# Optimization experiments

Hardware: AMD Instinct MI355X
Metric: run time of the kernel (lower is better)

Reference implementation:

```python
import jax, jax.numpy as jnp
import numpy as np


def setup_inputs() -> dict:
    key = jax.random.key(0)
    ks = jax.random.split(key, 8)
    N, E = 100000, 1600000
    d_in, d_h, d_out = 64, 128, 64
    x = jax.random.normal(ks[0], (N, d_in), dtype=jnp.float32)
    edge_index = jax.random.randint(ks[1], (2, E), 0, N, dtype=jnp.int64)
    def glorot(k, shape):
        lim = float(np.sqrt(6.0 / (shape[0] + shape[1])))
        return jax.random.uniform(k, shape, jnp.float32, -lim, lim)
    return {
        "x": x,
        "edge_index": edge_index,
        "W1": glorot(ks[2], (d_in, d_h)), "b1": jnp.zeros((d_h,), jnp.float32),
        "W2": glorot(ks[3], (d_h, d_h)), "b2": jnp.zeros((d_h,), jnp.float32),
        "W3": glorot(ks[4], (d_h, d_out)), "b3": jnp.zeros((d_out,), jnp.float32),
    }


def _gcn_norm(edge_index, num_nodes):
    # PyG gcn_norm with add_self_loops=True, edge_weight=1
    loops = jnp.arange(num_nodes, dtype=edge_index.dtype)
    src = jnp.concatenate([edge_index[0], loops])
    dst = jnp.concatenate([edge_index[1], loops])
    deg = jax.ops.segment_sum(jnp.ones_like(dst, dtype=jnp.float32), dst,
                              num_segments=num_nodes)
    dis = jnp.where(deg > 0, jax.lax.rsqrt(deg), 0.0)
    norm = dis[src] * dis[dst]  # [E+N]
    return src, dst, norm


def _gcn_layer(h, src, dst, norm, W, b, num_nodes):
    h = h @ W                                   # [N, d_out]
    msg = h[src] * norm[:, None]                # gather + scale
    out = jax.ops.segment_sum(msg, dst, num_segments=num_nodes)
    return out + b


def reference(x, edge_index, W1, b1, W2, b2, W3, b3):
    N = x.shape[0]
    src, dst, norm = _gcn_norm(edge_index, N)
    h = _gcn_layer(x, src, dst, norm, W1, b1, N)
    h = jax.nn.gelu(h, approximate=False)
    h = _gcn_layer(h, src, dst, norm, W2, b2, N)
    h = jax.nn.gelu(h, approximate=False)
    h = _gcn_layer(h, src, dst, norm, W3, b3, N)
    return h
```

## Files before the change

kernel.cpp:

```cpp
#include <hip/hip_runtime.h>
#include <hip/hip_fp16.h>
#include <cstdint>
#include <cstddef>


#define CHUNK 4096
#define BSHIFT 7
#define BSZ 128

typedef _Float16 half8 __attribute__((ext_vector_type(8)));
typedef float floatx4 __attribute__((ext_vector_type(4)));

__device__ __forceinline__ int eload(const int* ei, int elem, int is64) {
  return is64 ? ei[2 * elem] : ei[elem];
}

__global__ void k_detect(const int* __restrict__ ei, int* __restrict__ flag) {
  __shared__ int sh[256];
  int tid = threadIdx.x;
  int o = 0;
  for (int i = tid; i < 1024; i += 256) o |= ei[2 * i + 1];
  sh[tid] = o;
  __syncthreads();
  for (int s = 128; s > 0; s >>= 1) {
    if (tid < s) sh[tid] |= sh[tid + s];
    __syncthreads();
  }
  if (tid == 0) *flag = (sh[0] == 0) ? 1 : 0;
}

__global__ __launch_bounds__(256) void k_hist(const int* __restrict__ ei,
                                              int* __restrict__ hist, int E,
                                              int N, int NBLK,
                                              const int* __restrict__ flag) {
  __shared__ int lh[1024];
  int tid = threadIdx.x;
  int P = (N + BSZ - 1) >> BSHIFT;
  for (int i = tid; i < P; i += 256) lh[i] = 0;
  __syncthreads();
  int is64 = *flag;
  int e0 = blockIdx.x * CHUNK;
  int e1 = min(e0 + CHUNK, E);
  for (int e = e0 + tid; e < e1; e += 256) {
    int d = eload(ei, E + e, is64);
    atomicAdd(&lh[d >> BSHIFT], 1);
  }
  __syncthreads();
  for (int b = tid; b < P; b += 256) hist[b * NBLK + blockIdx.x] = lh[b];
}

__global__ __launch_bounds__(256) void k_scanA(const int* __restrict__ in,
                                               int* __restrict__ out,
                                               int* __restrict__ bsum, int n) {
  __shared__ int sh[256];
  int tid = threadIdx.x;
  int base = blockIdx.x * 1024 + tid * 4;
  int v0 = (base + 0 < n) ? in[base + 0] : 0;
  int v1 = (base + 1 < n) ? in[base + 1] : 0;
  int v2 = (base + 2 < n) ? in[base + 2] : 0;
  int v3 = (base + 3 < n) ? in[base + 3] : 0;
  int tsum = v0 + v1 + v2 + v3;
  sh[tid] = tsum;
  __syncthreads();
  for (int o = 1; o < 256; o <<= 1) {
    int x = (tid >= o) ? sh[tid - o] : 0;
    __syncthreads();
    sh[tid] += x;
    __syncthreads();
  }
  int excl = sh[tid] - tsum;
  if (base + 0 < n) out[base + 0] = excl;
  if (base + 1 < n) out[base + 1] = excl + v0;
  if (base + 2 < n) out[base + 2] = excl + v0 + v1;
  if (base + 3 < n) out[base + 3] = excl + v0 + v1 + v2;
  if (tid == 255) bsum[blockIdx.x] = sh[255];
}

__global__ __launch_bounds__(256) void k_scanB(int* __restrict__ bsum, int NB) {
  __shared__ int sh[256];
  int tid = threadIdx.x;
  int base = tid * 4;
  int v0 = (base + 0 < NB) ? bsum[base + 0] : 0;
  int v1 = (base + 1 < NB) ? bsum[base + 1] : 0;
  int v2 = (base + 2 < NB) ? bsum[base + 2] : 0;
  int v3 = (base + 3 < NB) ? bsum[base + 3] : 0;
  int tsum = v0 + v1 + v2 + v3;
  sh[tid] = tsum;
  __syncthreads();
  for (int o = 1; o < 256; o <<= 1) {
    int x = (tid >= o) ? sh[tid - o] : 0;
    __syncthreads();
    sh[tid] += x;
    __syncthreads();
  }
  int excl = sh[tid] - tsum;
  if (base + 0 < NB) bsum[base + 0] = excl;
  if (base + 1 < NB) bsum[base + 1] = excl + v0;
  if (base + 2 < NB) bsum[base + 2] = excl + v0 + v1;
  if (base + 3 < NB) bsum[base + 3] = excl + v0 + v1 + v2;
}

__global__ __launch_bounds__(256) void k_scanC(int* __restrict__ out,
                                               const int* __restrict__ bsum,
                                               int n, int total) {
  int i = blockIdx.x * 256 + threadIdx.x;
  if (i == 0) out[n] = total;
  if (i < n) out[i] += bsum[i >> 10];
}

__global__ __launch_bounds__(256) void k_scatter(const int* __restrict__ ei,
                                                 const int* __restrict__ histoff,
                                                 int* __restrict__ pairs, int E,
                                                 int N, int NBLK,
                                                 const int* __restrict__ flag) {
  __shared__ int lcur[1024];
  int tid = threadIdx.x;
  int P = (N + BSZ - 1) >> BSHIFT;
  for (int b = tid; b < P; b += 256)
    lcur[b] = histoff[b * NBLK + blockIdx.x];
  __syncthreads();
  int is64 = *flag;
  int e0 = blockIdx.x * CHUNK;
  int e1 = min(e0 + CHUNK, E);
  for (int e = e0 + tid; e < e1; e += 256) {
    int s = eload(ei, e, is64);
    int d = eload(ei, E + e, is64);
    int pos = atomicAdd(&lcur[d >> BSHIFT], 1);
    pairs[pos] = (s << BSHIFT) | (d & (BSZ - 1));
  }
}

__global__ __launch_bounds__(256) void k_build_bucket(
    const int* __restrict__ pairs, const int* __restrict__ histoff,
    int* __restrict__ off, float* __restrict__ dis, int* __restrict__ csr,
    int E, int N, int NBLK, int P) {
  __shared__ int lc[BSZ];
  __shared__ int lscan[BSZ];
  __shared__ int lcur[BSZ];
  int tid = threadIdx.x;
  int b = blockIdx.x;
  if (tid < BSZ) lc[tid] = 0;
  __syncthreads();
  int s0 = histoff[b * NBLK];
  int s1 = histoff[(b + 1) * NBLK];
  for (int i = s0 + tid; i < s1; i += 256)
    atomicAdd(&lc[pairs[i] & (BSZ - 1)], 1);
  __syncthreads();
  if (tid < BSZ) lscan[tid] = lc[tid];
  __syncthreads();
#pragma unroll
  for (int o = 1; o < BSZ; o <<= 1) {
    int v = 0;
    if (tid < BSZ && tid >= o) v = lscan[tid - o];
    __syncthreads();
    if (tid < BSZ) lscan[tid] += v;
    __syncthreads();
  }
  int node = (b << BSHIFT) + tid;
  if (tid < BSZ) {
    int o_node = s0 + lscan[tid] - lc[tid];
    lcur[tid] = o_node;
    if (node < N) {
      off[node] = o_node;
      dis[node] = rsqrtf((float)(lc[tid] + 1));
    }
  }
  if (b == P - 1 && tid == 0) off[N] = E;
  __syncthreads();
  for (int i = s0 + tid; i < s1; i += 256) {
    int pk = pairs[i];
    int pos = atomicAdd(&lcur[pk & (BSZ - 1)], 1);
    csr[pos] = pk >> BSHIFT;
  }
}

__global__ __launch_bounds__(256) void k_scale(const float* __restrict__ x,
                                               const float* __restrict__ dis,
                                               __half* __restrict__ xs, int N) {
  int i = blockIdx.x * 256 + threadIdx.x;
  int total = N * 16;
  if (i < total) {
    float d = dis[i >> 4];
    float4 v = ((const float4*)x)[i];
    union { uint2 u; __half2 h[2]; } pk;
    pk.h[0] = __floats2half2_rn(v.x * d, v.y * d);
    pk.h[1] = __floats2half2_rn(v.z * d, v.w * d);
    ((uint2*)xs)[i] = pk.u;
  }
}

__device__ __forceinline__ float gelu_exact(float v) {
  return 0.5f * v * (1.0f + erff(v * 0.70710678118654752440f));
}

template <int K, int M, int EPI>
__global__ __launch_bounds__(256) void k_gemm5(
    const __half* __restrict__ X, const float* __restrict__ W,
    const float* __restrict__ dis, const float* __restrict__ bias,
    __half* __restrict__ G, int N) {
  constexpr int NT = M / 16;
  constexpr int KK = K / 32;
  __shared__ _Float16 WtL[M * K];

  int tid = threadIdx.x;
  for (int t = tid; t < M * K / 8; t += 256) {
    int l = t & 63;
    int fid = t >> 6;
    int nt = fid / KK, kk = fid % KK;
    int n = nt * 16 + (l & 15);
    int k0 = kk * 32 + (l >> 4) * 8;
    half8 h;
#pragma unroll
    for (int e = 0; e < 8; e++)
      h[e] = (_Float16)W[(size_t)(k0 + e) * M + n];
    *(half8*)&WtL[(size_t)t * 8] = h;
  }
  __syncthreads();

  int wave = tid >> 6, l = tid & 63;
  int lr = l & 15, lg = l >> 4;
  int row0 = blockIdx.x * 64 + wave * 16;

  half8 a[KK];
  {
    int row = min(row0 + lr, N - 1);
    const __half* xp = X + (size_t)row * K + lg * 8;
#pragma unroll
    for (int kk = 0; kk < KK; kk++)
      a[kk] = *(const half8*)(xp + kk * 32);
  }

  floatx4 acc[NT];
#pragma unroll
  for (int nt = 0; nt < NT; nt++) acc[nt] = {0.f, 0.f, 0.f, 0.f};

#pragma unroll
  for (int nt = 0; nt < NT; nt++) {
#pragma unroll
    for (int kk = 0; kk < KK; kk++) {
      half8 b = *(const half8*)&WtL[(size_t)((nt * KK + kk) * 64 + l) * 8];
      acc[nt] = __builtin_amdgcn_mfma_f32_16x16x32_f16(a[kk], b, acc[nt], 0, 0, 0);
    }
  }

#pragma unroll
  for (int r = 0; r < 4; r++) {
    int row = row0 + lg * 4 + r;
    if (row < N) {
      float dd = (EPI == 0) ? dis[row] : 0.f;
#pragma unroll
      for (int nt = 0; nt < NT; nt++) {
        int col = nt * 16 + lr;
        float v = acc[nt][r];
        if constexpr (EPI == 0) v *= dd;
        else v = gelu_exact(v + bias[col]);
        G[(size_t)row * M + col] = __float2half(v);
      }
    }
  }
}

__device__ __forceinline__ void acc8(float* a, uint4 r) {
  const __half2* h = reinterpret_cast<const __half2*>(&r);
#pragma unroll
  for (int q = 0; q < 4; q++) {
    float2 f = __half22float2(h[q]);
    a[2 * q] += f.x;
    a[2 * q + 1] += f.y;
  }
}

template <int D, bool HAS_BIAS, bool HAS_GELU, bool F16OUT>
__global__ __launch_bounds__(256) void k_agg(
    const __half* __restrict__ g, const int* __restrict__ off,
    const int* __restrict__ csr, const float* __restrict__ dis,
    const float* __restrict__ bias, void* __restrict__ outv, int N) {
  constexpr int LPN = D / 8;
  constexpr int NPW = 64 / LPN;
  int wave = (blockIdx.x * 256 + threadIdx.x) >> 6;
  int lane = threadIdx.x & 63;
  int sub = lane / LPN;
  int sl = lane % LPN;
  int node = wave * NPW + sub;
  if (node >= N) return;
  const uint4* G16 = (const uint4*)g;
  float a[8];
#pragma unroll
  for (int q = 0; q < 8; q++) a[q] = 0.f;
  acc8(a, G16[(size_t)node * LPN + sl]);
  int beg = off[node], end = off[node + 1];
  int j = beg;
  for (; j + 4 <= end; j += 4) {
    int s0 = csr[j], s1 = csr[j + 1], s2 = csr[j + 2], s3 = csr[j + 3];
    uint4 r0 = G16[(size_t)s0 * LPN + sl];
    uint4 r1 = G16[(size_t)s1 * LPN + sl];
    uint4 r2 = G16[(size_t)s2 * LPN + sl];
    uint4 r3 = G16[(size_t)s3 * LPN + sl];
    acc8(a, r0);
    acc8(a, r1);
    acc8(a, r2);
    acc8(a, r3);
  }
  for (; j < end; j++) acc8(a, G16[(size_t)csr[j] * LPN + sl]);
  float dd = dis[node];
  int c0 = sl * 8;
  float v[8];
#pragma unroll
  for (int q = 0; q < 8; q++) v[q] = a[q] * dd;
  if constexpr (HAS_BIAS) {
    float4 b0 = *(const float4*)&bias[c0];
    float4 b1 = *(const float4*)&bias[c0 + 4];
    v[0] += b0.x; v[1] += b0.y; v[2] += b0.z; v[3] += b0.w;
    v[4] += b1.x; v[5] += b1.y; v[6] += b1.z; v[7] += b1.w;
  }
  if constexpr (HAS_GELU) {
#pragma unroll
    for (int q = 0; q < 8; q++) v[q] = gelu_exact(v[q]);
  }
  if constexpr (F16OUT) {
    union { uint4 u; __half2 h[4]; } pk;
#pragma unroll
    for (int q = 0; q < 4; q++)
      pk.h[q] = __floats2half2_rn(v[2 * q], v[2 * q + 1]);
    *(uint4*)&((__half*)outv)[(size_t)node * D + c0] = pk.u;
  } else {
    float* out = (float*)outv;
    float4 o0 = {v[0], v[1], v[2], v[3]};
    float4 o1 = {v[4], v[5], v[6], v[7]};
    *(float4*)&out[(size_t)node * D + c0] = o0;
    *(float4*)&out[(size_t)node * D + c0 + 4] = o1;
  }
}

extern "C" void kernel_launch(void* const* d_in, const int* in_sizes, int n_in,
                              void* d_out, int out_size, void* d_ws,
                              size_t ws_size, hipStream_t stream) {
  const float* x = (const float*)d_in[0];
  const int* ei = (const int*)d_in[1];
  const float* W1 = (const float*)d_in[2];
  const float* b1 = (const float*)d_in[3];
  const float* W2 = (const float*)d_in[4];
  const float* b2 = (const float*)d_in[5];
  const float* W3 = (const float*)d_in[6];
  const float* b3 = (const float*)d_in[7];
  float* out = (float*)d_out;

  const int N = in_sizes[0] / 64;
  const int E = in_sizes[1] / 2;

  const int NBLK = (E + CHUNK - 1) / CHUNK;
  const int P = (N + BSZ - 1) >> BSHIFT;
  const int HT = P * NBLK;

  char* p = (char*)d_ws;
  auto alloc = [&](size_t bytes) {
    char* r = p;
    p += (bytes + 255) & ~(size_t)255;
    return r;
  };
  float* dis = (float*)alloc((size_t)N * 4);
  int* off = (int*)alloc((size_t)(N + 1) * 4);
  int* bsumH = (int*)alloc(4096);
  int* flag = (int*)alloc(256);
  int* hist = (int*)alloc((size_t)(HT + 1) * 4);
  int* histoff = (int*)alloc((size_t)(HT + 1) * 4);
  int* pairs = (int*)alloc((size_t)E * 4);
  int* csr = (int*)alloc((size_t)E * 4);
  __half* xsh = (__half*)alloc((size_t)N * 64 * 2);
  __half* Xa_h = (__half*)alloc((size_t)N * 64 * 2);
  __half* h1_h = (__half*)alloc((size_t)N * 128 * 2);
  __half* gh = (__half*)alloc((size_t)N * 128 * 2);
  __half* h2_h = (__half*)alloc((size_t)N * 128 * 2);
  __half* gh2 = (__half*)alloc((size_t)N * 64 * 2);

  const int NBH = (HT + 1023) / 1024;

  k_detect<<<1, 256, 0, stream>>>(ei, flag);
  k_hist<<<NBLK, 256, 0, stream>>>(ei, hist, E, N, NBLK, flag);
  k_scanA<<<NBH, 256, 0, stream>>>(hist, histoff, bsumH, HT);
  k_scanB<<<1, 256, 0, stream>>>(bsumH, NBH);
  k_scanC<<<(HT + 255) / 256, 256, 0, stream>>>(histoff, bsumH, HT, E);
  k_scatter<<<NBLK, 256, 0, stream>>>(ei, histoff, pairs, E, N, NBLK, flag);
  k_build_bucket<<<P, 256, 0, stream>>>(pairs, histoff, off, dis, csr, E, N,
                                        NBLK, P);

  const int gemm_blocks = (N + 63) / 64;
  const int agg128_blocks = (N + 15) / 16;
  const int agg64_blocks = (N + 31) / 32;

  k_scale<<<(N * 16 + 255) / 256, 256, 0, stream>>>(x, dis, xsh, N);
  k_agg<64, false, false, true><<<agg64_blocks, 256, 0, stream>>>(
      xsh, off, csr, dis, nullptr, (void*)Xa_h, N);
  k_gemm5<64, 128, 1><<<gemm_blocks, 256, 0, stream>>>(Xa_h, W1, nullptr, b1,
                                                       h1_h, N);
  k_gemm5<128, 128, 0><<<gemm_blocks, 256, 0, stream>>>(h1_h, W2, dis, nullptr,
                                                        gh, N);
  k_agg<128, true, true, true><<<agg128_blocks, 256, 0, stream>>>(
      gh, off, csr, dis, b2, (void*)h2_h, N);
  k_gemm5<128, 64, 0><<<gemm_blocks, 256, 0, stream>>>(h2_h, W3, dis, nullptr,
                                                       gh2, N);
  k_agg<64, true, false, false><<<agg64_blocks, 256, 0, stream>>>(
      gh2, off, csr, dis, b3, (void*)out, N);
}
```

Baseline: 235.3 us.

## Replace histogram scan chain with atomic bucket offsets and per-block int64 detection

```diff
diff --git a/kernel.cpp b/kernel.cpp
--- a/kernel.cpp
+++ b/kernel.cpp
@@ -15,50 +15,53 @@
   return is64 ? ei[2 * elem] : ei[elem];
 }
 
-__global__ void k_detect(const int* __restrict__ ei, int* __restrict__ flag) {
-  __shared__ int sh[256];
-  int tid = threadIdx.x;
-  int o = 0;
-  for (int i = tid; i < 1024; i += 256) o |= ei[2 * i + 1];
-  sh[tid] = o;
-  __syncthreads();
-  for (int s = 128; s > 0; s >>= 1) {
-    if (tid < s) sh[tid] |= sh[tid + s];
-    __syncthreads();
-  }
-  if (tid == 0) *flag = (sh[0] == 0) ? 1 : 0;
-}
-
-__global__ __launch_bounds__(256) void k_hist(const int* __restrict__ ei,
-                                              int* __restrict__ hist, int E,
-                                              int N, int NBLK,
-                                              const int* __restrict__ flag) {
+__device__ __forceinline__ int detect_is64(const int* ei, int e0, int e1,
+                                           int* lflag) {
+  int tid = threadIdx.x;
+  if (tid == 0) *lflag = 0;
+  __syncthreads();
+  int cnt = min(256, e1 - e0);
+  if (tid < cnt) {
+    if (ei[2 * (e0 + tid) + 1] != 0) atomicOr(lflag, 1);
+  }
+  __syncthreads();
+  return (*lflag == 0) ? 1 : 0;
+}
+
+__global__ __launch_bounds__(256) void k_count(const int* __restrict__ ei,
+                                               int* __restrict__ total,
+                                               int* __restrict__ base_mat,
+                                               int E, int N, int NBLK) {
   __shared__ int lh[1024];
+  __shared__ int lflag;
   int tid = threadIdx.x;
   int P = (N + BSZ - 1) >> BSHIFT;
-  for (int i = tid; i < P; i += 256) lh[i] = 0;
-  __syncthreads();
-  int is64 = *flag;
   int e0 = blockIdx.x * CHUNK;
   int e1 = min(e0 + CHUNK, E);
+  int is64 = detect_is64(ei, e0, e1, &lflag);
+  for (int i = tid; i < P; i += 256) lh[i] = 0;
+  __syncthreads();
   for (int e = e0 + tid; e < e1; e += 256) {
     int d = eload(ei, E + e, is64);
     atomicAdd(&lh[d >> BSHIFT], 1);
   }
   __syncthreads();
-  for (int b = tid; b < P; b += 256) hist[b * NBLK + blockIdx.x] = lh[b];
-}
-
-__global__ __launch_bounds__(256) void k_scanA(const int* __restrict__ in,
-                                               int* __restrict__ out,
-                                               int* __restrict__ bsum, int n) {
+  for (int b = tid; b < P; b += 256) {
+    int c = lh[b];
+    base_mat[(size_t)b * NBLK + blockIdx.x] = c ? atomicAdd(&total[b], c) : 0;
+  }
+}
+
+__global__ __launch_bounds__(256) void k_scanP(const int* __restrict__ total,
+                                               int* __restrict__ base, int P,
+                                               int E) {
   __shared__ int sh[256];
   int tid = threadIdx.x;
-  int base = blockIdx.x * 1024 + tid * 4;
-  int v0 = (base + 0 < n) ? in[base + 0] : 0;
-  int v1 = (base + 1 < n) ? in[base + 1] : 0;
-  int v2 = (base + 2 < n) ? in[base + 2] : 0;
-  int v3 = (base + 3 < n) ? in[base + 3] : 0;
+  int b0 = tid * 4;
+  int v0 = (b0 + 0 < P) ? total[b0 + 0] : 0;
+  int v1 = (b0 + 1 < P) ? total[b0 + 1] : 0;
+  int v2 = (b0 + 2 < P) ? total[b0 + 2] : 0;
+  int v3 = (b0 + 3 < P) ? total[b0 + 3] : 0;
   int tsum = v0 + v1 + v2 + v3;
   sh[tid] = tsum;
   __syncthreads();
@@ -69,59 +72,27 @@
     __syncthreads();
   }
   int excl = sh[tid] - tsum;
-  if (base + 0 < n) out[base + 0] = excl;
-  if (base + 1 < n) out[base + 1] = excl + v0;
-  if (base + 2 < n) out[base + 2] = excl + v0 + v1;
-  if (base + 3 < n) out[base + 3] = excl + v0 + v1 + v2;
-  if (tid == 255) bsum[blockIdx.x] = sh[255];
-}
-
-__global__ __launch_bounds__(256) void k_scanB(int* __restrict__ bsum, int NB) {
-  __shared__ int sh[256];
-  int tid = threadIdx.x;
-  int base = tid * 4;
-  int v0 = (base + 0 < NB) ? bsum[base + 0] : 0;
-  int v1 = (base + 1 < NB) ? bsum[base + 1] : 0;
-  int v2 = (base + 2 < NB) ? bsum[base + 2] : 0;
-  int v3 = (base + 3 < NB) ? bsum[base + 3] : 0;
-  int tsum = v0 + v1 + v2 + v3;
-  sh[tid] = tsum;
-  __syncthreads();
-  for (int o = 1; o < 256; o <<= 1) {
-    int x = (tid >= o) ? sh[tid - o] : 0;
-    __syncthreads();
-    sh[tid] += x;
-    __syncthreads();
-  }
-  int excl = sh[tid] - tsum;
-  if (base + 0 < NB) bsum[base + 0] = excl;
-  if (base + 1 < NB) bsum[base + 1] = excl + v0;
-  if (base + 2 < NB) bsum[base + 2] = excl + v0 + v1;
-  if (base + 3 < NB) bsum[base + 3] = excl + v0 + v1 + v2;
-}
-
-__global__ __launch_bounds__(256) void k_scanC(int* __restrict__ out,
-                                               const int* __restrict__ bsum,
-                                               int n, int total) {
-  int i = blockIdx.x * 256 + threadIdx.x;
-  if (i == 0) out[n] = total;
-  if (i < n) out[i] += bsum[i >> 10];
-}
-
-__global__ __launch_bounds__(256) void k_scatter(const int* __restrict__ ei,
-                                                 const int* __restrict__ histoff,
-                                                 int* __restrict__ pairs, int E,
-                                                 int N, int NBLK,
-                                                 const int* __restrict__ flag) {
+  if (b0 + 0 < P) base[b0 + 0] = excl;
+  if (b0 + 1 < P) base[b0 + 1] = excl + v0;
+  if (b0 + 2 < P) base[b0 + 2] = excl + v0 + v1;
+  if (b0 + 3 < P) base[b0 + 3] = excl + v0 + v1 + v2;
+  if (tid == 0) base[P] = E;
+}
+
+__global__ __launch_bounds__(256) void k_scatter2(
+    const int* __restrict__ ei, const int* __restrict__ base,
+    const int* __restrict__ base_mat, int* __restrict__ pairs, int E, int N,
+    int NBLK) {
   __shared__ int lcur[1024];
+  __shared__ int lflag;
   int tid = threadIdx.x;
   int P = (N + BSZ - 1) >> BSHIFT;
-  for (int b = tid; b < P; b += 256)
-    lcur[b] = histoff[b * NBLK + blockIdx.x];
-  __syncthreads();
-  int is64 = *flag;
   int e0 = blockIdx.x * CHUNK;
   int e1 = min(e0 + CHUNK, E);
+  int is64 = detect_is64(ei, e0, e1, &lflag);
+  for (int b = tid; b < P; b += 256)
+    lcur[b] = base[b] + base_mat[(size_t)b * NBLK + blockIdx.x];
+  __syncthreads();
   for (int e = e0 + tid; e < e1; e += 256) {
     int s = eload(ei, e, is64);
     int d = eload(ei, E + e, is64);
@@ -131,9 +102,9 @@
 }
 
 __global__ __launch_bounds__(256) void k_build_bucket(
-    const int* __restrict__ pairs, const int* __restrict__ histoff,
+    const int* __restrict__ pairs, const int* __restrict__ base,
     int* __restrict__ off, float* __restrict__ dis, int* __restrict__ csr,
-    int E, int N, int NBLK, int P) {
+    int E, int N, int P) {
   __shared__ int lc[BSZ];
   __shared__ int lscan[BSZ];
   __shared__ int lcur[BSZ];
@@ -141,8 +112,8 @@
   int b = blockIdx.x;
   if (tid < BSZ) lc[tid] = 0;
   __syncthreads();
-  int s0 = histoff[b * NBLK];
-  int s1 = histoff[(b + 1) * NBLK];
+  int s0 = base[b];
+  int s1 = base[b + 1];
   for (int i = s0 + tid; i < s1; i += 256)
     atomicAdd(&lc[pairs[i] & (BSZ - 1)], 1);
   __syncthreads();
@@ -350,7 +321,6 @@
 
   const int NBLK = (E + CHUNK - 1) / CHUNK;
   const int P = (N + BSZ - 1) >> BSHIFT;
-  const int HT = P * NBLK;
 
   char* p = (char*)d_ws;
   auto alloc = [&](size_t bytes) {
@@ -360,10 +330,9 @@
   };
   float* dis = (float*)alloc((size_t)N * 4);
   int* off = (int*)alloc((size_t)(N + 1) * 4);
-  int* bsumH = (int*)alloc(4096);
-  int* flag = (int*)alloc(256);
-  int* hist = (int*)alloc((size_t)(HT + 1) * 4);
-  int* histoff = (int*)alloc((size_t)(HT + 1) * 4);
+  int* total = (int*)alloc((size_t)P * 4);
+  int* base = (int*)alloc((size_t)(P + 1) * 4);
+  int* base_mat = (int*)alloc((size_t)P * NBLK * 4);
   int* pairs = (int*)alloc((size_t)E * 4);
   int* csr = (int*)alloc((size_t)E * 4);
   __half* xsh = (__half*)alloc((size_t)N * 64 * 2);
@@ -373,16 +342,11 @@
   __half* h2_h = (__half*)alloc((size_t)N * 128 * 2);
   __half* gh2 = (__half*)alloc((size_t)N * 64 * 2);
 
-  const int NBH = (HT + 1023) / 1024;
-
-  k_detect<<<1, 256, 0, stream>>>(ei, flag);
-  k_hist<<<NBLK, 256, 0, stream>>>(ei, hist, E, N, NBLK, flag);
-  k_scanA<<<NBH, 256, 0, stream>>>(hist, histoff, bsumH, HT);
-  k_scanB<<<1, 256, 0, stream>>>(bsumH, NBH);
-  k_scanC<<<(HT + 255) / 256, 256, 0, stream>>>(histoff, bsumH, HT, E);
-  k_scatter<<<NBLK, 256, 0, stream>>>(ei, histoff, pairs, E, N, NBLK, flag);
-  k_build_bucket<<<P, 256, 0, stream>>>(pairs, histoff, off, dis, csr, E, N,
-                                        NBLK, P);
+  hipMemsetAsync(total, 0, (size_t)P * 4, stream);
+  k_count<<<NBLK, 256, 0, stream>>>(ei, total, base_mat, E, N, NBLK);
+  k_scanP<<<1, 256, 0, stream>>>(total, base, P, E);
+  k_scatter2<<<NBLK, 256, 0, stream>>>(ei, base, base_mat, pairs, E, N, NBLK);
+  k_build_bucket<<<P, 256, 0, stream>>>(pairs, base, off, dis, csr, E, N, P);
 
   const int gemm_blocks = (N + 63) / 64;
   const int agg128_blocks = (N + 15) / 16;
```

After: 242.1 us. +2.9%, slower.
